# Performance work log

Hardware: AMD Instinct MI355X
Metric: run time of the kernel (lower is better)

## Reference

```python
import jax, jax.numpy as jnp
import numpy as np

DN = ('NHWC', 'HWIO', 'NHWC')
BN_EPS = 1e-3  # Keras BatchNormalization default


def _conv(x, w, pad):
    return jax.lax.conv_general_dilated(x, w, (1, 1), pad, dimension_numbers=DN)


def _bn(x, p):
    # p: [4, C] rows = (gamma, beta, moving_mean, moving_var), inference mode
    g, b, m, v = p[0], p[1], p[2], p[3]
    return g * (x - m) * jax.lax.rsqrt(v + BN_EPS) + b


def _hard_swish(x):
    return x * jnp.clip(x + 3.0, 0.0, 6.0) * (1.0 / 6.0)


def _conv_block(x, w, bn_p, pad):
    # Conv module: ZeroPad+Conv2D(no bias) -> BN -> hard_swish
    return _hard_swish(_bn(_conv(x, w, pad), bn_p))


def setup_inputs() -> dict:
    key = jax.random.key(0)
    ks = jax.random.split(key, 17)
    s = 0.05  # keep activations numerically tame
    inp = {
        'x': jax.random.normal(ks[0], (16, 160, 160, 128), jnp.float32),
        'cv1_w': jax.random.normal(ks[1], (1, 1, 128, 64), jnp.float32) * s,
        'cv1_bn': jax.random.uniform(ks[2], (4, 64), jnp.float32),
        'm0_cv1_w': jax.random.normal(ks[3], (1, 1, 64, 64), jnp.float32) * s,
        'm0_cv1_bn': jax.random.uniform(ks[4], (4, 64), jnp.float32),
        'm0_cv2_w': jax.random.normal(ks[5], (3, 3, 64, 64), jnp.float32) * s,
        'm0_cv2_bn': jax.random.uniform(ks[6], (4, 64), jnp.float32),
        'm1_cv1_w': jax.random.normal(ks[7], (1, 1, 64, 64), jnp.float32) * s,
        'm1_cv1_bn': jax.random.uniform(ks[8], (4, 64), jnp.float32),
        'm1_cv2_w': jax.random.normal(ks[9], (3, 3, 64, 64), jnp.float32) * s,
        'm1_cv2_bn': jax.random.uniform(ks[10], (4, 64), jnp.float32),
        'cv3_w': jax.random.normal(ks[11], (1, 1, 64, 64), jnp.float32) * s,
        'cv2p_w': jax.random.normal(ks[12], (1, 1, 128, 64), jnp.float32) * s,
        'bn_cat': jax.random.uniform(ks[13], (4, 128), jnp.float32),
        'cv4_w': jax.random.normal(ks[14], (1, 1, 128, 128), jnp.float32) * s,
        'cv4_bn': jax.random.uniform(ks[15], (4, 128), jnp.float32),
    }
    return inp


def reference(x, cv1_w, cv1_bn, m0_cv1_w, m0_cv1_bn, m0_cv2_w, m0_cv2_bn,
              m1_cv1_w, m1_cv1_bn, m1_cv2_w, m1_cv2_bn,
              cv3_w, cv2p_w, bn_cat, cv4_w, cv4_bn):
    # BottleneckCSP(filters=128, n=2, shortcut=True, expansion=0.5)
    y = _conv_block(x, cv1_w, cv1_bn, 'VALID')            # cv1: 1x1 -> mid=64
    # m: 2 standard Bottlenecks(mid, mid, shortcut=True, expansion=1.0)
    for w1, p1, w2, p2 in ((m0_cv1_w, m0_cv1_bn, m0_cv2_w, m0_cv2_bn),
                           (m1_cv1_w, m1_cv1_bn, m1_cv2_w, m1_cv2_bn)):
        h = _conv_block(y, w1, p1, 'VALID')               # 1x1
        h = _conv_block(h, w2, p2, 'SAME')                # 3x3 (pad=1)
        y = y + h                                         # residual add
    x1 = _conv(y, cv3_w, 'VALID')                         # plain 1x1 conv, no BN/act
    x2 = _conv(x, cv2p_w, 'VALID')                        # plain 1x1 conv on input
    xc = jnp.concatenate([x1, x2], axis=-1)               # [B,H,W,128]
    xc = _bn(xc, bn_cat)
    xc = jnp.where(xc >= 0, xc, 0.1 * xc)                 # LeakyReLU(0.1)
    out = _conv_block(xc, cv4_w, cv4_bn, 'VALID')         # cv4: 1x1 -> 128
    return out
```

## Files before the change

kernel.cpp:

```cpp
#include <hip/hip_runtime.h>
#include <hip/hip_bf16.h>

using bf16   = __bf16;
using bf16x8 = __attribute__((ext_vector_type(8))) __bf16;
using bf16x4 = __attribute__((ext_vector_type(4))) __bf16;
using f32x4  = __attribute__((ext_vector_type(4))) float;

#define MFMA16(W, X, C) __builtin_amdgcn_mfma_f32_16x16x32_bf16((W), (X), (C), 0, 0, 0)

static constexpr size_t M_TOT = (size_t)16 * 160 * 160;

static constexpr size_t O_CV1  = 0;
static constexpr size_t O_CV2P = 8192;
static constexpr size_t O_M0C1 = 16384;
static constexpr size_t O_M0C2 = 20480;
static constexpr size_t O_M1C1 = 57344;
static constexpr size_t O_M1C2 = 61440;
static constexpr size_t O_CV3  = 98304;
static constexpr size_t O_CV4  = 102400;

__device__ __forceinline__ float hsw(float x) {
    return x * fminf(fmaxf(x + 3.f, 0.f), 6.f) * (1.f / 6.f);
}
__device__ __forceinline__ float lrelu(float x) {
    return x >= 0.f ? x : 0.1f * x;
}
__device__ __forceinline__ bf16x8 zero8() {
    bf16x8 t;
#pragma unroll
    for (int b = 0; b < 8; ++b) t[b] = (bf16)0.f;
    return t;
}
__device__ __forceinline__ f32x4 zero4f() {
    f32x4 t = {0.f, 0.f, 0.f, 0.f};
    return t;
}

template <int KTOT, int COUT>
__device__ void prep_w(bf16* __restrict__ dst, const float* __restrict__ W,
                       int gid, int gs) {
    constexpr int NKS = KTOT / 32, NCT = COUT / 16;
    for (int idx = gid; idx < NKS * NCT * 64; idx += gs) {
        int lane = idx & 63;
        int f = idx >> 6;
        int ct = f % NCT, ks = f / NCT;
        int j = ct * 16 + (lane & 15);
        int kb = ks * 32 + ((lane >> 4) << 3);
        bf16x8 t;
#pragma unroll
        for (int b = 0; b < 8; ++b) t[b] = (bf16)W[(size_t)(kb + b) * COUT + j];
        *(bf16x8*)(dst + (size_t)idx * 8) = t;
    }
}

__device__ void prep_bn(float* __restrict__ dst, const float* __restrict__ p,
                        int C, int off, int n, int gid, int gs) {
    for (int c = gid; c < n; c += gs) {
        float g = p[off + c], b = p[C + off + c];
        float m = p[2 * C + off + c], v = p[3 * C + off + c];
        float s = g * rsqrtf(v + 1e-3f);
        dst[c] = s;
        dst[128 + c] = b - m * s;
    }
}

__global__ __launch_bounds__(256) void k_prep(
    const float* __restrict__ w1, const float* __restrict__ w2p,
    const float* __restrict__ m0c1w, const float* __restrict__ m0c2w,
    const float* __restrict__ m1c1w, const float* __restrict__ m1c2w,
    const float* __restrict__ cv3w, const float* __restrict__ cv4w,
    const float* __restrict__ bn1, const float* __restrict__ bncat,
    const float* __restrict__ m0c1b, const float* __restrict__ m0c2b,
    const float* __restrict__ m1c1b, const float* __restrict__ m1c2b,
    const float* __restrict__ bn4, bf16* __restrict__ wb, float* __restrict__ bnb) {
    int gid = blockIdx.x * 256 + threadIdx.x;
    int gs = gridDim.x * 256;
    prep_w<128, 64>(wb + O_CV1, w1, gid, gs);
    prep_w<128, 64>(wb + O_CV2P, w2p, gid, gs);
    prep_w<64, 64>(wb + O_M0C1, m0c1w, gid, gs);
    prep_w<576, 64>(wb + O_M0C2, m0c2w, gid, gs);
    prep_w<64, 64>(wb + O_M1C1, m1c1w, gid, gs);
    prep_w<576, 64>(wb + O_M1C2, m1c2w, gid, gs);
    prep_w<64, 64>(wb + O_CV3, cv3w, gid, gs);
    prep_w<128, 128>(wb + O_CV4, cv4w, gid, gs);
    prep_bn(bnb + 0 * 256, bn1, 64, 0, 64, gid, gs);
    prep_bn(bnb + 1 * 256, bncat, 128, 64, 64, gid, gs);
    prep_bn(bnb + 2 * 256, m0c1b, 64, 0, 64, gid, gs);
    prep_bn(bnb + 3 * 256, m0c2b, 64, 0, 64, gid, gs);
    prep_bn(bnb + 4 * 256, m1c1b, 64, 0, 64, gid, gs);
    prep_bn(bnb + 5 * 256, m1c2b, 64, 0, 64, gid, gs);
    prep_bn(bnb + 6 * 256, bncat, 128, 0, 64, gid, gs);
    prep_bn(bnb + 7 * 256, bn4, 128, 0, 128, gid, gs);
}

__global__ __launch_bounds__(256, 3) void k_head(
    const float* __restrict__ x, const bf16* __restrict__ wa,
    const bf16* __restrict__ wbq, const float* __restrict__ bna,
    const float* __restrict__ bnb, bf16* __restrict__ y, bf16* __restrict__ x2) {
    int tid = threadIdx.x;
    int lane = tid & 63, wid = tid >> 6;
    int lr = lane & 15, lg = lane >> 4;
    int m0 = blockIdx.x * 128 + wid * 32;

    f32x4 accy[2][4], accx[2][4];
#pragma unroll
    for (int rt = 0; rt < 2; ++rt)
#pragma unroll
        for (int ct = 0; ct < 4; ++ct) { accy[rt][ct] = zero4f(); accx[rt][ct] = zero4f(); }

#pragma unroll
    for (int ks = 0; ks < 4; ++ks) {
        bf16x8 xa[2];
#pragma unroll
        for (int rt = 0; rt < 2; ++rt) {
            const float* p = x + (size_t)(m0 + rt * 16 + lr) * 128 + ks * 32 + lg * 8;
            f32x4 v0 = *(const f32x4*)p;
            f32x4 v1 = *(const f32x4*)(p + 4);
            bf16x8 t;
#pragma unroll
            for (int b = 0; b < 4; ++b) { t[b] = (bf16)v0[b]; t[b + 4] = (bf16)v1[b]; }
            xa[rt] = t;
        }
#pragma unroll
        for (int ct = 0; ct < 4; ++ct) {
            bf16x8 fa = *(const bf16x8*)(wa + (size_t)((ks * 4 + ct) * 64 + lane) * 8);
            bf16x8 fb = *(const bf16x8*)(wbq + (size_t)((ks * 4 + ct) * 64 + lane) * 8);
#pragma unroll
            for (int rt = 0; rt < 2; ++rt) {
                accy[rt][ct] = MFMA16(fa, xa[rt], accy[rt][ct]);
                accx[rt][ct] = MFMA16(fb, xa[rt], accx[rt][ct]);
            }
        }
    }
#pragma unroll
    for (int rt = 0; rt < 2; ++rt) {
        size_t r = (size_t)(m0 + rt * 16 + lr);
#pragma unroll
        for (int ct = 0; ct < 4; ++ct) {
            int j0 = ct * 16 + lg * 4;
            f32x4 s4 = *(const f32x4*)(bna + j0), h4 = *(const f32x4*)(bna + 128 + j0);
            f32x4 a = accy[rt][ct];
            bf16x4 oy, ox;
#pragma unroll
            for (int b = 0; b < 4; ++b) oy[b] = (bf16)hsw(a[b] * s4[b] + h4[b]);
            *(bf16x4*)(y + r * 64 + j0) = oy;
            s4 = *(const f32x4*)(bnb + j0);
            h4 = *(const f32x4*)(bnb + 128 + j0);
            a = accx[rt][ct];
#pragma unroll
            for (int b = 0; b < 4; ++b) ox[b] = (bf16)lrelu(a[b] * s4[b] + h4[b]);
            *(bf16x4*)(x2 + r * 64 + j0) = ox;
        }
    }
}

__global__ __launch_bounds__(256, 4) void k_cb64(
    const bf16* __restrict__ in, const bf16* __restrict__ wg,
    const float* __restrict__ bnp, bf16* __restrict__ out) {
    int tid = threadIdx.x;
    int lane = tid & 63, wid = tid >> 6;
    int lr = lane & 15, lg = lane >> 4;
    bf16x8 wf[2][4];
#pragma unroll
    for (int ks = 0; ks < 2; ++ks)
#pragma unroll
        for (int ct = 0; ct < 4; ++ct)
            wf[ks][ct] = *(const bf16x8*)(wg + (size_t)((ks * 4 + ct) * 64 + lane) * 8);

    int m0 = blockIdx.x * 256 + wid * 64;
    f32x4 acc[4][4];
#pragma unroll
    for (int rt = 0; rt < 4; ++rt)
#pragma unroll
        for (int ct = 0; ct < 4; ++ct) acc[rt][ct] = zero4f();

#pragma unroll
    for (int ks = 0; ks < 2; ++ks) {
        bf16x8 xa[4];
#pragma unroll
        for (int rt = 0; rt < 4; ++rt)
            xa[rt] = *(const bf16x8*)(in + (size_t)(m0 + rt * 16 + lr) * 64 + ks * 32 + lg * 8);
#pragma unroll
        for (int ct = 0; ct < 4; ++ct)
#pragma unroll
            for (int rt = 0; rt < 4; ++rt)
                acc[rt][ct] = MFMA16(wf[ks][ct], xa[rt], acc[rt][ct]);
    }
#pragma unroll
    for (int rt = 0; rt < 4; ++rt) {
        size_t r = (size_t)(m0 + rt * 16 + lr);
#pragma unroll
        for (int ct = 0; ct < 4; ++ct) {
            int j0 = ct * 16 + lg * 4;
            f32x4 s4 = *(const f32x4*)(bnp + j0), h4 = *(const f32x4*)(bnp + 128 + j0);
            f32x4 a = acc[rt][ct];
            bf16x4 o;
#pragma unroll
            for (int b = 0; b < 4; ++b) o[b] = (bf16)hsw(a[b] * s4[b] + h4[b]);
            *(bf16x4*)(out + r * 64 + j0) = o;
        }
    }
}

__global__ __launch_bounds__(256, 3) void k_c3(
    const bf16* __restrict__ in, const bf16* __restrict__ wg,
    const float* __restrict__ bnp, bf16* __restrict__ y) {
    int tid = threadIdx.x;
    int lane = tid & 63;
    int lr = lane & 15, lg = lane >> 4;
    int m0 = blockIdx.x * 256 + (tid >> 6) * 64;

    int row[4], wc[4], hr[4];
#pragma unroll
    for (int rt = 0; rt < 4; ++rt) {
        int r = m0 + rt * 16 + lr;
        row[rt] = r;
        int q = r / 160;
        wc[rt] = r - q * 160;
        hr[rt] = q % 160;
    }
    f32x4 acc[4][4];
#pragma unroll
    for (int rt = 0; rt < 4; ++rt)
#pragma unroll
        for (int ct = 0; ct < 4; ++ct) acc[rt][ct] = zero4f();

    const bf16* wl = wg + (size_t)lane * 8;

#pragma unroll
    for (int tap = 0; tap < 9; ++tap) {
        const int dy = tap / 3 - 1, dx = tap % 3 - 1;
        const int roff = dy * 160 + dx;
#pragma unroll
        for (int ks2 = 0; ks2 < 2; ++ks2) {
            int ks = tap * 2 + ks2;
            bf16x8 xa[4];
#pragma unroll
            for (int rt = 0; rt < 4; ++rt) {
                bool v = ((unsigned)(hr[rt] + dy) < 160u) && ((unsigned)(wc[rt] + dx) < 160u);
                bf16x8 t = zero8();
                if (v)
                    t = *(const bf16x8*)(in + (size_t)(row[rt] + roff) * 64 + ks2 * 32 + lg * 8);
                xa[rt] = t;
            }
            bf16x8 wfr[4];
#pragma unroll
            for (int ct = 0; ct < 4; ++ct)
                wfr[ct] = *(const bf16x8*)(wl + (size_t)((ks * 4 + ct) * 64) * 8);
#pragma unroll
            for (int ct = 0; ct < 4; ++ct)
#pragma unroll
                for (int rt = 0; rt < 4; ++rt)
                    acc[rt][ct] = MFMA16(wfr[ct], xa[rt], acc[rt][ct]);
        }
    }
#pragma unroll
    for (int rt = 0; rt < 4; ++rt) {
        size_t r = (size_t)row[rt];
#pragma unroll
        for (int ct = 0; ct < 4; ++ct) {
            int j0 = ct * 16 + lg * 4;
            f32x4 s4 = *(const f32x4*)(bnp + j0), h4 = *(const f32x4*)(bnp + 128 + j0);
            f32x4 a = acc[rt][ct];
            bf16x4 old = *(const bf16x4*)(y + r * 64 + j0);
            bf16x4 o;
#pragma unroll
            for (int b = 0; b < 4; ++b)
                o[b] = (bf16)((float)old[b] + hsw(a[b] * s4[b] + h4[b]));
            *(bf16x4*)(y + r * 64 + j0) = o;
        }
    }
}

__global__ __launch_bounds__(256, 3) void k_tail(
    const bf16* __restrict__ y, const bf16* __restrict__ x2,
    const bf16* __restrict__ w3g, const bf16* __restrict__ w4g,
    const float* __restrict__ bnlo, const float* __restrict__ bn4,
    float* __restrict__ out) {
    __shared__ bf16 tl[4 * 32 * 64];
    int tid = threadIdx.x;
    int lane = tid & 63, wid = tid >> 6;
    int lr = lane & 15, lg = lane >> 4;
    int m0 = blockIdx.x * 128 + wid * 32;
    char* tlw = (char*)(tl + (size_t)wid * 32 * 64);

    f32x4 a1[2][4];
#pragma unroll
    for (int rt = 0; rt < 2; ++rt)
#pragma unroll
        for (int ct = 0; ct < 4; ++ct) a1[rt][ct] = zero4f();
#pragma unroll
    for (int ks = 0; ks < 2; ++ks) {
        bf16x8 xa[2];
#pragma unroll
        for (int rt = 0; rt < 2; ++rt)
            xa[rt] = *(const bf16x8*)(y + (size_t)(m0 + rt * 16 + lr) * 64 + ks * 32 + lg * 8);
#pragma unroll
        for (int ct = 0; ct < 4; ++ct) {
            bf16x8 wfr = *(const bf16x8*)(w3g + (size_t)((ks * 4 + ct) * 64 + lane) * 8);
#pragma unroll
            for (int rt = 0; rt < 2; ++rt) a1[rt][ct] = MFMA16(wfr, xa[rt], a1[rt][ct]);
        }
    }
#pragma unroll
    for (int rt = 0; rt < 2; ++rt) {
        int rr = rt * 16 + lr;
#pragma unroll
        for (int ct = 0; ct < 4; ++ct) {
            int j0 = ct * 16 + lg * 4;
            f32x4 s4 = *(const f32x4*)(bnlo + j0), h4 = *(const f32x4*)(bnlo + 128 + j0);
            f32x4 a = a1[rt][ct];
            bf16x4 o;
#pragma unroll
            for (int b = 0; b < 4; ++b) o[b] = (bf16)lrelu(a[b] * s4[b] + h4[b]);
            int byo = (rr * 128 + j0 * 2) ^ ((rr & 7) << 4);
            *(bf16x4*)(tlw + byo) = o;
        }
    }
    __syncthreads();

    f32x4 a2[2][8];
#pragma unroll
    for (int rt = 0; rt < 2; ++rt)
#pragma unroll
        for (int ct = 0; ct < 8; ++ct) a2[rt][ct] = zero4f();
#pragma unroll
    for (int ks = 0; ks < 4; ++ks) {
        bf16x8 xa[2];
        if (ks < 2) {
#pragma unroll
            for (int rt = 0; rt < 2; ++rt) {
                int rr = rt * 16 + lr;
                int byo = (rr * 128 + (ks * 32 + lg * 8) * 2) ^ ((rr & 7) << 4);
                xa[rt] = *(const bf16x8*)(tlw + byo);
            }
        } else {
#pragma unroll
            for (int rt = 0; rt < 2; ++rt)
                xa[rt] = *(const bf16x8*)(x2 + (size_t)(m0 + rt * 16 + lr) * 64 +
                                          (ks - 2) * 32 + lg * 8);
        }
#pragma unroll
        for (int ct = 0; ct < 8; ++ct) {
            bf16x8 wfr = *(const bf16x8*)(w4g + (size_t)((ks * 8 + ct) * 64 + lane) * 8);
#pragma unroll
            for (int rt = 0; rt < 2; ++rt) a2[rt][ct] = MFMA16(wfr, xa[rt], a2[rt][ct]);
        }
    }
#pragma unroll
    for (int rt = 0; rt < 2; ++rt) {
        size_t r = (size_t)(m0 + rt * 16 + lr);
#pragma unroll
        for (int ct = 0; ct < 8; ++ct) {
            int j0 = ct * 16 + lg * 4;
            f32x4 s4 = *(const f32x4*)(bn4 + j0), h4 = *(const f32x4*)(bn4 + 128 + j0);
            f32x4 a = a2[rt][ct];
            f32x4 o;
#pragma unroll
            for (int b = 0; b < 4; ++b) o[b] = hsw(a[b] * s4[b] + h4[b]);
            *(f32x4*)(out + r * 128 + j0) = o;
        }
    }
}

extern "C" void kernel_launch(void* const* d_in, const int* in_sizes, int n_in,
                              void* d_out, int out_size, void* d_ws, size_t ws_size,
                              hipStream_t stream) {
    const float* x      = (const float*)d_in[0];
    const float* cv1_w  = (const float*)d_in[1];
    const float* cv1_bn = (const float*)d_in[2];
    const float* m0c1w  = (const float*)d_in[3];
    const float* m0c1b  = (const float*)d_in[4];
    const float* m0c2w  = (const float*)d_in[5];
    const float* m0c2b  = (const float*)d_in[6];
    const float* m1c1w  = (const float*)d_in[7];
    const float* m1c1b  = (const float*)d_in[8];
    const float* m1c2w  = (const float*)d_in[9];
    const float* m1c2b  = (const float*)d_in[10];
    const float* cv3_w  = (const float*)d_in[11];
    const float* cv2p_w = (const float*)d_in[12];
    const float* bn_cat = (const float*)d_in[13];
    const float* cv4_w  = (const float*)d_in[14];
    const float* cv4_bn = (const float*)d_in[15];
    float* out = (float*)d_out;

    const size_t M = M_TOT;
    bf16* y  = (bf16*)d_ws;
    bf16* x2 = y + M * 64;
    bf16* h  = x2 + M * 64;
    bf16* wb = h + M * 64;
    float* bnb = (float*)(wb + 120832);

    dim3 blk(256);
    k_prep<<<dim3(64), blk, 0, stream>>>(cv1_w, cv2p_w, m0c1w, m0c2w, m1c1w, m1c2w,
                                         cv3_w, cv4_w, cv1_bn, bn_cat, m0c1b, m0c2b,
                                         m1c1b, m1c2b, cv4_bn, wb, bnb);
    k_head<<<dim3((int)(M / 128)), blk, 0, stream>>>(
        x, wb + O_CV1, wb + O_CV2P, bnb + 0 * 256, bnb + 1 * 256, y, x2);
    k_cb64<<<dim3((int)(M / 256)), blk, 0, stream>>>(y, wb + O_M0C1, bnb + 2 * 256, h);
    k_c3 <<<dim3((int)(M / 256)), blk, 0, stream>>>(h, wb + O_M0C2, bnb + 3 * 256, y);
    k_cb64<<<dim3((int)(M / 256)), blk, 0, stream>>>(y, wb + O_M1C1, bnb + 4 * 256, h);
    k_c3 <<<dim3((int)(M / 256)), blk, 0, stream>>>(h, wb + O_M1C2, bnb + 5 * 256, y);
    k_tail<<<dim3((int)(M / 128)), blk, 0, stream>>>(
        y, x2, wb + O_CV3, wb + O_CV4, bnb + 6 * 256, bnb + 7 * 256, out);
}
```

Before: 753.8 us.

## Stage 3x3 conv halo tile and 1x1 weights in shared memory

The 3x3 conv kernel now loads a block's 256 rows plus a 161-row halo on each side into a swizzled LDS tile once. All nine taps then read from LDS instead of issuing repeated global loads. The head and tail kernels copy their weight matrices into LDS before the MFMA loops, and launch bounds change to 4 for head and 2 for the conv kernel. The halo load is unconditional, so the first and last blocks read outside the activation buffer before those values are masked out. The larger LDS footprint also lowers occupancy.

```diff
diff --git a/kernel.cpp b/kernel.cpp
--- a/kernel.cpp
+++ b/kernel.cpp
@@ -93,11 +93,17 @@
     prep_bn(bnb + 7 * 256, bn4, 128, 0, 128, gid, gs);
 }
 
-__global__ __launch_bounds__(256, 3) void k_head(
+__global__ __launch_bounds__(256, 4) void k_head(
     const float* __restrict__ x, const bf16* __restrict__ wa,
     const bf16* __restrict__ wbq, const float* __restrict__ bna,
     const float* __restrict__ bnb, bf16* __restrict__ y, bf16* __restrict__ x2) {
+    __shared__ bf16 wa_l[8192], wb_l[8192];
     int tid = threadIdx.x;
+    for (int i = tid; i < 1024; i += 256) {
+        *(bf16x8*)(wa_l + (size_t)i * 8) = *(const bf16x8*)(wa + (size_t)i * 8);
+        *(bf16x8*)(wb_l + (size_t)i * 8) = *(const bf16x8*)(wbq + (size_t)i * 8);
+    }
+    __syncthreads();
     int lane = tid & 63, wid = tid >> 6;
     int lr = lane & 15, lg = lane >> 4;
     int m0 = blockIdx.x * 128 + wid * 32;
@@ -123,8 +129,8 @@
         }
 #pragma unroll
         for (int ct = 0; ct < 4; ++ct) {
-            bf16x8 fa = *(const bf16x8*)(wa + (size_t)((ks * 4 + ct) * 64 + lane) * 8);
-            bf16x8 fb = *(const bf16x8*)(wbq + (size_t)((ks * 4 + ct) * 64 + lane) * 8);
+            bf16x8 fa = *(const bf16x8*)(wa_l + (size_t)((ks * 4 + ct) * 64 + lane) * 8);
+            bf16x8 fb = *(const bf16x8*)(wb_l + (size_t)((ks * 4 + ct) * 64 + lane) * 8);
 #pragma unroll
             for (int rt = 0; rt < 2; ++rt) {
                 accy[rt][ct] = MFMA16(fa, xa[rt], accy[rt][ct]);
@@ -202,15 +208,27 @@
     }
 }
 
-__global__ __launch_bounds__(256, 3) void k_c3(
+__global__ __launch_bounds__(256, 2) void k_c3(
     const bf16* __restrict__ in, const bf16* __restrict__ wg,
     const float* __restrict__ bnp, bf16* __restrict__ y) {
+    constexpr int NR = 578;
+    __shared__ bf16 tile[NR * 64];
     int tid = threadIdx.x;
-    int lane = tid & 63;
+    const long g0 = (long)blockIdx.x * 256 - 161;
+    const char* inb = (const char*)in;
+
+    for (int i = tid; i < NR * 8; i += 256) {
+        int row_l = i >> 3, c = i & 7;
+        bf16x8 v = *(const bf16x8*)(inb + (g0 + row_l) * 128 + ((c ^ (row_l & 7)) << 4));
+        *(bf16x8*)((char*)tile + (size_t)i * 16) = v;
+    }
+    __syncthreads();
+
+    int lane = tid & 63, wid = tid >> 6;
     int lr = lane & 15, lg = lane >> 4;
-    int m0 = blockIdx.x * 256 + (tid >> 6) * 64;
-
-    int row[4], wc[4], hr[4];
+    int m0 = blockIdx.x * 256 + wid * 64;
+
+    int row[4], wc[4], hr[4], lbase[4];
 #pragma unroll
     for (int rt = 0; rt < 4; ++rt) {
         int r = m0 + rt * 16 + lr;
@@ -218,6 +236,7 @@
         int q = r / 160;
         wc[rt] = r - q * 160;
         hr[rt] = q % 160;
+        lbase[rt] = wid * 64 + rt * 16 + lr + 161;
     }
     f32x4 acc[4][4];
 #pragma unroll
@@ -237,11 +256,11 @@
             bf16x8 xa[4];
 #pragma unroll
             for (int rt = 0; rt < 4; ++rt) {
+                int row_l = lbase[rt] + roff;
+                bf16x8 t = *(const bf16x8*)((const char*)tile + (size_t)row_l * 128 +
+                                            ((((ks2 << 2) | lg) ^ (row_l & 7)) << 4));
                 bool v = ((unsigned)(hr[rt] + dy) < 160u) && ((unsigned)(wc[rt] + dx) < 160u);
-                bf16x8 t = zero8();
-                if (v)
-                    t = *(const bf16x8*)(in + (size_t)(row[rt] + roff) * 64 + ks2 * 32 + lg * 8);
-                xa[rt] = t;
+                xa[rt] = v ? t : zero8();
             }
             bf16x8 wfr[4];
 #pragma unroll
@@ -277,8 +296,15 @@
     const bf16* __restrict__ w3g, const bf16* __restrict__ w4g,
     const float* __restrict__ bnlo, const float* __restrict__ bn4,
     float* __restrict__ out) {
+    __shared__ bf16 w3l[4096];
+    __shared__ bf16 w4l[16384];
     __shared__ bf16 tl[4 * 32 * 64];
     int tid = threadIdx.x;
+    for (int i = tid; i < 512; i += 256)
+        *(bf16x8*)(w3l + (size_t)i * 8) = *(const bf16x8*)(w3g + (size_t)i * 8);
+    for (int i = tid; i < 2048; i += 256)
+        *(bf16x8*)(w4l + (size_t)i * 8) = *(const bf16x8*)(w4g + (size_t)i * 8);
+    __syncthreads();
     int lane = tid & 63, wid = tid >> 6;
     int lr = lane & 15, lg = lane >> 4;
     int m0 = blockIdx.x * 128 + wid * 32;
@@ -297,7 +323,7 @@
             xa[rt] = *(const bf16x8*)(y + (size_t)(m0 + rt * 16 + lr) * 64 + ks * 32 + lg * 8);
 #pragma unroll
         for (int ct = 0; ct < 4; ++ct) {
-            bf16x8 wfr = *(const bf16x8*)(w3g + (size_t)((ks * 4 + ct) * 64 + lane) * 8);
+            bf16x8 wfr = *(const bf16x8*)(w3l + (size_t)((ks * 4 + ct) * 64 + lane) * 8);
 #pragma unroll
             for (int rt = 0; rt < 2; ++rt) a1[rt][ct] = MFMA16(wfr, xa[rt], a1[rt][ct]);
         }
@@ -342,7 +368,7 @@
         }
 #pragma unroll
         for (int ct = 0; ct < 8; ++ct) {
-            bf16x8 wfr = *(const bf16x8*)(w4g + (size_t)((ks * 8 + ct) * 64 + lane) * 8);
+            bf16x8 wfr = *(const bf16x8*)(w4l + (size_t)((ks * 8 + ct) * 64 + lane) * 8);
 #pragma unroll
             for (int rt = 0; rt < 2; ++rt) a2[rt][ct] = MFMA16(wfr, xa[rt], a2[rt][ct]);
         }
```

Result: faster. 736.2 us (-2.3%).
